# Optimization experiments

Measured on AMD Instinct MI355X. Metric: run time of the kernel, lower is better.

Reference implementation:

```python
import jax, jax.numpy as jnp
import numpy as np

D = 1024; H = 16; K = 64; BK = 32; FFN = 4096; LORA = 48; CHUNK = 64
THETA_CLIP = float(np.pi / 2)
THETA_INIT = float(np.pi / 16)


def layernorm(x, g, b, eps=1e-6):
    m = x.mean(-1, keepdims=True)
    v = ((x - m) ** 2).mean(-1, keepdims=True)
    return (x - m) * jax.lax.rsqrt(v + eps) * g + b


def setup_inputs() -> dict:
    key = jax.random.key(0)
    ks = jax.random.split(key, 24)
    w = lambda k, s: jax.random.normal(k, s, jnp.float32) * 0.02
    return {
        "x": jax.random.normal(ks[0], (4, 2048, D), jnp.float32),
        "Wq": w(ks[1], (D, D)), "bq": jnp.zeros((D,), jnp.float32),
        "Wk": w(ks[2], (D, D)), "bk": jnp.zeros((D,), jnp.float32),
        "Wv": w(ks[3], (D, D)), "bv": jnp.zeros((D,), jnp.float32),
        "Wo": w(ks[4], (D, D)), "bo": jnp.zeros((D,), jnp.float32),
        "n1g": jnp.ones((D,), jnp.float32), "n1b": jnp.zeros((D,), jnp.float32),
        "n2g": jnp.ones((D,), jnp.float32), "n2b": jnp.zeros((D,), jnp.float32),
        "theta_base": jax.random.uniform(ks[5], (H, BK), jnp.float32, -THETA_INIT, THETA_INIT),
        "theta_w1": w(ks[6], (D, LORA)),
        "theta_w2": jax.random.uniform(ks[7], (LORA, H * BK), jnp.float32, -0.01, 0.01),
        "lambda_base": jax.random.uniform(ks[8], (H, BK), jnp.float32, 0.5, 6.0),
        "eta": jax.random.normal(ks[9], (H, BK), jnp.float32) * 0.1,
        "Wf1": w(ks[10], (D, FFN)), "bf1": jnp.zeros((FFN,), jnp.float32),
        "Wf2": w(ks[11], (FFN, D)), "bf2": jnp.zeros((D,), jnp.float32),
    }


def _forward(x, Wq, bq, Wk, bk, Wv, bv, Wo, bo, n1g, n1b, n2g, n2b,
             theta_base, theta_w1, theta_w2, lambda_base, eta, Wf1, bf1, Wf2, bf2):
    B, T, _ = x.shape
    NC = T // CHUNK
    xn = layernorm(x, n1g, n1b)
    # projections -> (B, H, T, K)
    q = (xn @ Wq + bq).reshape(B, T, H, K).transpose(0, 2, 1, 3)
    k = (xn @ Wk + bk).reshape(B, T, H, K).transpose(0, 2, 1, 3)
    v = (xn @ Wv + bv).reshape(B, T, H, K).transpose(0, 2, 1, 3)
    phi_k = jnp.where(k > 0, k + 1.0, jnp.exp(k))  # elu(k) + 1
    qp = q.reshape(B, H, T, BK, 2)
    kp = phi_k.reshape(B, H, T, BK, 2)
    q_c = jax.lax.complex(qp[..., 0], qp[..., 1])  # (B,H,T,BK) complex64
    k_c = jax.lax.complex(kp[..., 0], kp[..., 1])
    # data-dependent rotation angles via LoRA
    lora = jnp.tanh(xn @ theta_w1) @ theta_w2  # (B,T,H*BK)
    theta = theta_base[None, None] + lora.reshape(B, T, H, BK)
    theta = jnp.clip(theta, -THETA_CLIP, THETA_CLIP).transpose(0, 2, 1, 3)  # (B,H,T,BK)
    lam = lambda_base[None, :, None, :] + eta[None, :, None, :] * theta ** 2
    log_z = jax.lax.complex(-lam, theta)  # complex log-decay per step

    def chunks(a):  # (B,H,T,...) -> (NC,B,H,CHUNK,...)
        return jnp.moveaxis(a.reshape(B, H, NC, CHUNK, *a.shape[3:]), 2, 0)

    tril = jnp.tril(jnp.ones((CHUNK, CHUNK), bool))[None, None, :, :, None]

    def step(c, inputs):
        lz, kc, qc, vf = inputs  # (B,H,tc,BK)x3, (B,H,tc,K)
        cumlog = jnp.cumsum(lz, axis=2)
        diff = cumlog[:, :, :, None, :] - cumlog[:, :, None, :, :]  # (B,H,tc,tc,BK)
        real = jnp.where(tril, diff.real, -60.0)
        A = jnp.where(tril, jnp.exp(jax.lax.complex(real, diff.imag)),
                      jnp.zeros((), jnp.complex64))
        scaled_k = A * kc[:, :, None, :, :]
        S_intra = jnp.einsum('bhtsk,bhsv->bhtkv', scaled_k, vf.astype(jnp.complex64))
        decay = jnp.exp(cumlog)
        S_total = decay[..., None] * c[:, :, None] + S_intra  # (B,H,tc,BK,K)
        y = jnp.einsum('bhtk,bhtkv->bhtv', jnp.conj(qc), S_total).real
        return S_total[:, :, -1], y

    c0 = jnp.zeros((B, H, BK, K), jnp.complex64)
    _, ys = jax.lax.scan(step, c0, (chunks(log_z), chunks(k_c), chunks(q_c), chunks(v)))
    out = jnp.moveaxis(ys, 0, 2).reshape(B, H, T, K)
    attn = out.transpose(0, 2, 1, 3).reshape(B, T, D) @ Wo + bo
    x1 = x + attn
    h = layernorm(x1, n2g, n2b)
    return x1 + jax.nn.gelu(h @ Wf1 + bf1) @ Wf2 + bf2


def reference(x, Wq, bq, Wk, bk, Wv, bv, Wo, bo, n1g, n1b, n2g, n2b,
              theta_base, theta_w1, theta_w2, lambda_base, eta, Wf1, bf1, Wf2, bf2):
    return _forward(x, Wq, bq, Wk, bk, Wv, bv, Wo, bo, n1g, n1b, n2g, n2b,
                    theta_base, theta_w1, theta_w2, lambda_base, eta, Wf1, bf1, Wf2, bf2)
```

## Files before the change

### kernel.cpp

```cpp
#include <hip/hip_runtime.h>


typedef __bf16 bf16x8 __attribute__((ext_vector_type(8)));
typedef float f32x4 __attribute__((ext_vector_type(4)));

__device__ __forceinline__ unsigned short f2bf(float f) {
  unsigned int u = __builtin_bit_cast(unsigned int, f);
  u += 0x7FFFu + ((u >> 16) & 1u);
  return (unsigned short)(u >> 16);
}
__device__ __forceinline__ float bf2f(unsigned short u) {
  unsigned int x = ((unsigned int)u) << 16;
  return __builtin_bit_cast(float, x);
}
__device__ __forceinline__ unsigned int pack2(float a, float b) {
  return (unsigned int)f2bf(a) | ((unsigned int)f2bf(b) << 16);
}

__device__ __forceinline__ void gload_lds16(const void* g, void* l) {
  __builtin_amdgcn_global_load_lds((const __attribute__((address_space(1))) void*)g,
                                   (__attribute__((address_space(3))) void*)l, 16, 0, 0);
}

__device__ __forceinline__ float gelu_tanh(float v) {
  const float z = 0.7978845608028654f * fmaf(0.044715f * v * v, v, v);
  const float e = __expf(2.f * z);
  return 0.5f * v * (2.f - 2.f / (1.f + e));
}

__global__ void fill_kernel(float* p, float v, int n) {
  int i = blockIdx.x * 256 + threadIdx.x;
  if (i < n) p[i] = v;
}

__global__ __launch_bounds__(256) void ln_kernel(
    const float* __restrict__ x, const float* __restrict__ g,
    const float* __restrict__ b, unsigned short* __restrict__ out) {
  const int row = blockIdx.x, tid = threadIdx.x;
  float4 v = ((const float4*)(x + (size_t)row * 1024))[tid];
  float s = v.x + v.y + v.z + v.w;
  float sq = v.x * v.x + v.y * v.y + v.z * v.z + v.w * v.w;
#pragma unroll
  for (int o = 32; o > 0; o >>= 1) { s += __shfl_xor(s, o); sq += __shfl_xor(sq, o); }
  __shared__ float red[8];
  const int wid = tid >> 6;
  if ((tid & 63) == 0) { red[wid] = s; red[4 + wid] = sq; }
  __syncthreads();
  s = red[0] + red[1] + red[2] + red[3];
  sq = red[4] + red[5] + red[6] + red[7];
  const float mean = s * (1.f / 1024.f);
  const float var = sq * (1.f / 1024.f) - mean * mean;
  const float rstd = rsqrtf(var + 1e-6f);
  float4 gv = ((const float4*)g)[tid];
  float4 bvv = ((const float4*)b)[tid];
  ushort4 o4;
  o4.x = f2bf((v.x - mean) * rstd * gv.x + bvv.x);
  o4.y = f2bf((v.y - mean) * rstd * gv.y + bvv.y);
  o4.z = f2bf((v.z - mean) * rstd * gv.z + bvv.z);
  o4.w = f2bf((v.w - mean) * rstd * gv.w + bvv.w);
  *(ushort4*)(out + (size_t)row * 1024 + tid * 4) = o4;
}

__global__ __launch_bounds__(256) void transpose_bf16(
    const float* __restrict__ src, unsigned short* __restrict__ dst, int K, int N) {
  __shared__ float tile[32][33];
  const int n0 = blockIdx.x * 32, k0 = blockIdx.y * 32;
  const int tx = threadIdx.x, ty = threadIdx.y;
#pragma unroll
  for (int j = 0; j < 32; j += 8) tile[tx][ty + j] = src[(size_t)(k0 + ty + j) * N + n0 + tx];
  __syncthreads();
#pragma unroll
  for (int j = 0; j < 32; j += 8)
    dst[(size_t)(n0 + ty + j) * K + k0 + tx] = f2bf(tile[ty + j][tx]);
}

__global__ __launch_bounds__(256) void prep_wcat(
    const float* __restrict__ Wq, const float* __restrict__ Wk,
    const float* __restrict__ Wv, const float* __restrict__ tw1,
    unsigned short* __restrict__ dst) {
  __shared__ float tile[32][33];
  const int r0 = blockIdx.x * 32, c0 = blockIdx.y * 32;
  const int tx = threadIdx.x, ty = threadIdx.y;
  const int r = r0 + tx;
#pragma unroll
  for (int j = 0; j < 32; j += 8) {
    const int c = c0 + ty + j;
    float v;
    if (r < 1024) v = Wq[(size_t)c * 1024 + r];
    else if (r < 2048) v = Wk[(size_t)c * 1024 + (r - 1024)];
    else if (r < 3072) v = Wv[(size_t)c * 1024 + (r - 2048)];
    else if (r < 3120) v = tw1[(size_t)c * 48 + (r - 3072)];
    else v = 0.f;
    tile[tx][ty + j] = v;
  }
  __syncthreads();
#pragma unroll
  for (int j = 0; j < 32; j += 8)
    dst[(size_t)(r0 + ty + j) * 1024 + c0 + tx] = f2bf(tile[ty + j][tx]);
}

__global__ void biascat_kernel(const float* bq, const float* bk, const float* bv, float* dst) {
  int i = blockIdx.x * 256 + threadIdx.x;
  if (i >= 3200) return;
  float v = 0.f;
  if (i < 1024) v = bq[i];
  else if (i < 2048) v = bk[i - 1024];
  else if (i < 3072) v = bv[i - 2048];
  dst[i] = v;
}

template <int MODE>
__global__ __launch_bounds__(256) void gemm_kernel(
    const unsigned short* __restrict__ A, const unsigned short* __restrict__ BT,
    const float* __restrict__ bias, const float* __restrict__ res,
    void* __restrict__ out, int N, int Kd) {
  __shared__ unsigned short As[128 * 64];
  __shared__ unsigned short Bs[128 * 64];
  const int nwg = gridDim.x * gridDim.y;
  int d = blockIdx.y * gridDim.x + blockIdx.x;
  d = (d & 7) * (nwg >> 3) + (d >> 3);
  const int n0 = (d % gridDim.x) * 128, m0 = (d / gridDim.x) * 128;

  const int tid = threadIdx.x, wv = tid >> 6, ln = tid & 63;
  const int wm = wv >> 1, wn = wv & 1;
  const int l15 = ln & 15, hi4 = ln >> 4;
  const int rbase = wv * 8 + (ln >> 3);
  const int kgofs = ((ln & 7) ^ ((ln >> 3) & 7)) * 8;

  f32x4 acc[4][4] = {};
  for (int k0 = 0; k0 < Kd; k0 += 64) {
#pragma unroll
    for (int jj = 0; jj < 4; ++jj) {
      gload_lds16(A + (size_t)(m0 + jj * 32 + rbase) * Kd + k0 + kgofs,
                  (char*)As + (jj * 256 + wv * 64) * 16);
      gload_lds16(BT + (size_t)(n0 + jj * 32 + rbase) * Kd + k0 + kgofs,
                  (char*)Bs + (jj * 256 + wv * 64) * 16);
    }
    __syncthreads();
#pragma unroll
    for (int kk = 0; kk < 64; kk += 32) {
      const int kg = (kk >> 3) + hi4;
      bf16x8 av[4], bv[4];
#pragma unroll
      for (int f = 0; f < 4; ++f) {
        const int ra = wm * 64 + f * 16 + l15;
        const int rb2 = wn * 64 + f * 16 + l15;
        av[f] = *(const bf16x8*)&As[(ra * 8 + (kg ^ (ra & 7))) * 8];
        bv[f] = *(const bf16x8*)&Bs[(rb2 * 8 + (kg ^ (rb2 & 7))) * 8];
      }
#pragma unroll
      for (int fm = 0; fm < 4; ++fm)
#pragma unroll
        for (int fn = 0; fn < 4; ++fn)
          acc[fm][fn] = __builtin_amdgcn_mfma_f32_16x16x32_bf16(av[fm], bv[fn], acc[fm][fn], 0, 0, 0);
    }
    __syncthreads();
  }
  const int rb = hi4 * 4;
#pragma unroll
  for (int fm = 0; fm < 4; ++fm) {
#pragma unroll
    for (int fn = 0; fn < 4; ++fn) {
      const int row = m0 + wm * 64 + fm * 16 + rb;
      const int col = n0 + wn * 64 + fn * 16 + l15;
      const float bval = bias[col];
#pragma unroll
      for (int r = 0; r < 4; ++r) {
        float v = acc[fm][fn][r] + bval;
        const size_t oi = (size_t)(row + r) * N + col;
        if constexpr (MODE == 1) v += res[oi];
        if constexpr (MODE == 2) {
          ((unsigned short*)out)[oi] = f2bf(gelu_tanh(v));
        } else if constexpr (MODE == 3) {
          ((unsigned short*)out)[oi] = f2bf(v);
        } else {
          ((float*)out)[oi] = v;
        }
      }
    }
  }
}

__global__ __launch_bounds__(256) void lora2_kernel(
    const unsigned short* __restrict__ qkv, const float* __restrict__ w2,
    const float* __restrict__ tbase, float* __restrict__ theta) {
  __shared__ float lt[8][48];
  const int m0 = blockIdx.x * 32;
  const int tid = threadIdx.x;
  const int col = tid * 2;
  const float tb0 = tbase[col], tb1 = tbase[col + 1];
  for (int grp = 0; grp < 4; ++grp) {
    const int mg = m0 + grp * 8;
    __syncthreads();
    for (int idx = tid; idx < 384; idx += 256) {
      const int tok = idx / 48, jj = idx % 48;
      lt[tok][jj] = tanhf(bf2f(qkv[(size_t)(mg + tok) * 3200 + 3072 + jj]));
    }
    __syncthreads();
    float a0[8], a1[8];
#pragma unroll
    for (int tok = 0; tok < 8; ++tok) { a0[tok] = tb0; a1[tok] = tb1; }
    for (int jj = 0; jj < 48; ++jj) {
      const float2 w = *(const float2*)&w2[(size_t)jj * 512 + col];
#pragma unroll
      for (int tok = 0; tok < 8; ++tok) {
        const float l = lt[tok][jj];
        a0[tok] = fmaf(l, w.x, a0[tok]);
        a1[tok] = fmaf(l, w.y, a1[tok]);
      }
    }
    const float CL = 1.5707963267948966f;
#pragma unroll
    for (int tok = 0; tok < 8; ++tok) {
      float c0 = fminf(fmaxf(a0[tok], -CL), CL);
      float c1 = fminf(fmaxf(a1[tok], -CL), CL);
      *(float2*)&theta[(size_t)(mg + tok) * 512 + col] = make_float2(c0, c1);
    }
  }
}

__global__ __launch_bounds__(256) void attn_intra(
    const unsigned short* __restrict__ qkv, const float* __restrict__ theta,
    const float* __restrict__ lamb, const float* __restrict__ eta,
    float* __restrict__ yi, unsigned short* __restrict__ QG,
    unsigned short* __restrict__ TCG, float* __restrict__ Dg) {
  const int c = blockIdx.x, bh = blockIdx.y;
  const int b = bh >> 4, h = bh & 15;
  const int tid = threadIdx.x, wv = tid >> 6, lane = tid & 63;
  const int sc = c * 4 + wv;
  const int cid = bh * 128 + sc;
  const int mw = b * 2048 + sc * 16;

  __shared__ unsigned short QDm[4][16][64];
  __shared__ unsigned short KDm[4][16][64];
  __shared__ unsigned short KdET[4][64][32];
  __shared__ unsigned short VT[4][64][32];
  __shared__ unsigned short Gs[4][16][32];

  {
    unsigned int* kz = (unsigned int*)&KdET[wv][0][0];
    unsigned int* vz = (unsigned int*)&VT[wv][0][0];
    for (int idx = lane; idx < 512; idx += 64) {
      const int r = idx >> 3, p = (idx & 7) + 8;
      kz[r * 16 + p] = 0; vz[r * 16 + p] = 0;
    }
    unsigned int* gz = (unsigned int*)&Gs[wv][0][0];
    for (int idx = lane; idx < 128; idx += 64) {
      const int r = idx >> 3, p = (idx & 7) + 8;
      gz[r * 16 + p] = 0;
    }
  }
  for (int ss = 0; ss < 16; ++ss)
    VT[wv][lane][ss] = qkv[(size_t)(mw + ss) * 3200 + 2048 + h * 64 + lane];

  const int bk = lane & 31, th = lane >> 5;
  const float lb = lamb[h * 32 + bk], et = eta[h * 32 + bk];
  float L[8], Th[8], qr[8], qi[8], kr[8], ki[8];
  float runL = 0.f, runT = 0.f;
#pragma unroll
  for (int i = 0; i < 8; ++i) {
    const size_t m = (size_t)(mw + th * 8 + i);
    const float tv = theta[m * 512 + h * 32 + bk];
    const float lam = fmaf(et * tv, tv, lb);
    runL += lam; L[i] = runL;
    runT += tv;  Th[i] = runT;
    const unsigned int qp = *(const unsigned int*)&qkv[m * 3200 + h * 64 + 2 * bk];
    const unsigned int kp = *(const unsigned int*)&qkv[m * 3200 + 1024 + h * 64 + 2 * bk];
    qr[i] = bf2f((unsigned short)(qp & 0xFFFF)); qi[i] = bf2f((unsigned short)(qp >> 16));
    const float kx = bf2f((unsigned short)(kp & 0xFFFF));
    const float ky = bf2f((unsigned short)(kp >> 16));
    kr[i] = kx > 0.f ? kx + 1.f : __expf(kx);
    ki[i] = ky > 0.f ? ky + 1.f : __expf(ky);
  }
  const float oL = __shfl_xor(runL, 32), oT = __shfl_xor(runT, 32);
  const float Lm = th ? oL : runL;
  const float Tm = th ? oT : runT;
  const float Ltot = runL + oL, Ttot = runT + oT;
  const float Lbase = th ? oL : 0.f, Tbase = th ? oT : 0.f;
  float Es, Ec; __sincosf(Tm, &Es, &Ec);
  const float Ee = __expf(-Lm);
  const float Er = Ee * Ec, Ei = Ee * Es;
  float Fs, Fc; __sincosf(Ttot - Tm, &Fs, &Fc);
  const float Fe = __expf(-(Ltot - Lm));
  const float Fr = Fe * Fc, Fi = Fe * Fs;
  if (th == 0) {
    float Ds, Dc; __sincosf(Ttot, &Ds, &Dc);
    const float De = __expf(-Ltot);
    *(float2*)&Dg[((size_t)cid * 32 + bk) * 2] = make_float2(De * Dc, De * Ds);
  }
  unsigned int* qd32 = (unsigned int*)&QDm[wv][0][0];
  unsigned int* kd32 = (unsigned int*)&KDm[wv][0][0];
#pragma unroll
  for (int i = 0; i < 8; ++i) {
    const int t = th * 8 + i;
    const float Lg = Lbase + L[i], Tg = Tbase + Th[i];
    const float dm = __expf(-(Lg - Lm));
    float sn, cs; __sincosf(Tg - Tm, &sn, &cs);
    const float qmr = dm * (qr[i] * cs + qi[i] * sn);
    const float qmi = dm * (qr[i] * sn - qi[i] * cs);
    const float rd = 1.f / dm;
    const float kmr = rd * (kr[i] * cs + ki[i] * sn);
    const float kmi = rd * (ki[i] * cs - kr[i] * sn);
    const int sidx = (t * 32 + bk) ^ ((t & 7) << 2);
    qd32[sidx] = pack2(qmr, qmi);
    kd32[sidx] = pack2(kmr, -kmi);
    ((unsigned int*)QG)[(size_t)cid * 512 + t * 32 + bk] =
        pack2(qmr * Er - qmi * Ei, qmr * Ei + qmi * Er);
    const float er = kmr * Fr - kmi * Fi;
    const float ei = kmr * Fi + kmi * Fr;
    KdET[wv][bk][t] = f2bf(er);
    KdET[wv][32 + bk][t] = f2bf(ei);
  }

  const int l15 = lane & 15, hi = lane >> 4;
  const char* qb = (const char*)&QDm[wv][0][0];
  const char* kb = (const char*)&KDm[wv][0][0];
  f32x4 z = {};
  f32x4 g = z;
  {
    bf16x8 a0 = *(const bf16x8*)(qb + l15 * 128 + ((16 * hi) ^ ((l15 & 7) << 4)));
    bf16x8 b0 = *(const bf16x8*)(kb + l15 * 128 + ((16 * hi) ^ ((l15 & 7) << 4)));
    bf16x8 a1 = *(const bf16x8*)(qb + l15 * 128 + ((64 + 16 * hi) ^ ((l15 & 7) << 4)));
    bf16x8 b1 = *(const bf16x8*)(kb + l15 * 128 + ((64 + 16 * hi) ^ ((l15 & 7) << 4)));
    g = __builtin_amdgcn_mfma_f32_16x16x32_bf16(a0, b0, g, 0, 0, 0);
    g = __builtin_amdgcn_mfma_f32_16x16x32_bf16(a1, b1, g, 0, 0, 0);
  }
#pragma unroll
  for (int r = 0; r < 4; ++r) {
    const float gv = (l15 <= 4 * hi + r) ? g[r] : 0.f;
    Gs[wv][4 * hi + r][l15] = f2bf(gv);
  }
  const char* gsb = (const char*)&Gs[wv][0][0];
  const char* vtb = (const char*)&VT[wv][0][0];
  bf16x8 aG = *(const bf16x8*)(gsb + l15 * 64 + 16 * hi);
#pragma unroll
  for (int nt = 0; nt < 4; ++nt) {
    bf16x8 bV = *(const bf16x8*)(vtb + (nt * 16 + l15) * 64 + 16 * hi);
    f32x4 y = __builtin_amdgcn_mfma_f32_16x16x32_bf16(aG, bV, z, 0, 0, 0);
#pragma unroll
    for (int r = 0; r < 4; ++r)
      yi[(size_t)cid * 1024 + (4 * hi + r) * 64 + nt * 16 + l15] = y[r];
  }
  const char* keb = (const char*)&KdET[wv][0][0];
#pragma unroll
  for (int mt = 0; mt < 4; ++mt) {
    bf16x8 aT = *(const bf16x8*)(keb + (mt * 16 + l15) * 64 + 16 * hi);
#pragma unroll
    for (int nt = 0; nt < 4; ++nt) {
      bf16x8 bV = *(const bf16x8*)(vtb + (nt * 16 + l15) * 64 + 16 * hi);
      f32x4 t4 = __builtin_amdgcn_mfma_f32_16x16x32_bf16(aT, bV, z, 0, 0, 0);
#pragma unroll
      for (int r = 0; r < 4; ++r)
        TCG[(size_t)cid * 4096 + (mt * 16 + 4 * hi + r) * 64 + nt * 16 + l15] = f2bf(t4[r]);
    }
  }
}

__global__ __launch_bounds__(256) void scanB_kernel(
    const unsigned short* __restrict__ TCG, const float* __restrict__ Dg,
    unsigned int* __restrict__ CPACK) {
  const int bh = blockIdx.x & 63, g = blockIdx.x >> 6;
  const int tid = threadIdx.x;
  const int v = g * 8 + (tid >> 5), bk = tid & 31;
  const size_t base = (size_t)bh * 128;
  float Cr = 0.f, Ci = 0.f;
  float trx[4], tix[4]; float2 dx[4];
  auto LOADQ = [&](int c0, float* tr, float* ti, float2* dd) {
#pragma unroll
    for (int u = 0; u < 4; ++u) {
      const size_t cid = base + c0 + u;
      tr[u] = bf2f(TCG[cid * 4096 + bk * 64 + v]);
      ti[u] = bf2f(TCG[cid * 4096 + (32 + bk) * 64 + v]);
      dd[u] = *(const float2*)&Dg[(cid * 32 + bk) * 2];
    }
  };
  LOADQ(0, trx, tix, dx);
  for (int c0 = 0; c0 < 128; c0 += 4) {
    float tra[4], tia[4]; float2 da[4];
#pragma unroll
    for (int u = 0; u < 4; ++u) { tra[u] = trx[u]; tia[u] = tix[u]; da[u] = dx[u]; }
    if (c0 + 4 < 128) LOADQ(c0 + 4, trx, tix, dx);
#pragma unroll
    for (int u = 0; u < 4; ++u) {
      CPACK[(base + c0 + u) * 2048 + v * 32 + bk] = pack2(Cr, -Ci);
      const float nr = fmaf(da[u].x, Cr, fmaf(-da[u].y, Ci, tra[u]));
      const float ni = fmaf(da[u].x, Ci, fmaf(da[u].y, Cr, tia[u]));
      Cr = nr; Ci = ni;
    }
  }
}

__global__ __launch_bounds__(256) void attn_cross(
    const float* __restrict__ yi, const unsigned short* __restrict__ QG,
    const unsigned int* __restrict__ CPACK, unsigned short* __restrict__ attn) {
  const int c = blockIdx.x, bh = blockIdx.y;
  const int b = bh >> 4, h = bh & 15;
  const int tid = threadIdx.x, wv = tid >> 6, lane = tid & 63;
  const int sc = c * 4 + wv, cid = bh * 128 + sc;
  const int mw = b * 2048 + sc * 16;
  __shared__ unsigned short Cp[4][64][64];
  __shared__ unsigned short Qs[4][16][64];
  unsigned int* cp32 = (unsigned int*)&Cp[wv][0][0];
  const unsigned int* cg = CPACK + (size_t)cid * 2048;
  for (int ii = 0; ii < 32; ++ii) {
    const int flat = ii * 64 + lane;
    const int row = flat >> 5, col = flat & 31;
    cp32[(row * 32 + col) ^ ((row & 7) << 2)] = cg[flat];
  }
  unsigned int* qs32 = (unsigned int*)&Qs[wv][0][0];
  const unsigned int* qg = (const unsigned int*)QG + (size_t)cid * 512;
  for (int ii = 0; ii < 8; ++ii) {
    const int flat = ii * 64 + lane;
    const int row = flat >> 5, col = flat & 31;
    qs32[(row * 32 + col) ^ ((row & 7) << 2)] = qg[flat];
  }
  const int l15 = lane & 15, hi = lane >> 4;
  const char* qb = (const char*)&Qs[wv][0][0];
  const char* cb = (const char*)&Cp[wv][0][0];
  bf16x8 a0 = *(const bf16x8*)(qb + l15 * 128 + ((16 * hi) ^ ((l15 & 7) << 4)));
  bf16x8 a1 = *(const bf16x8*)(qb + l15 * 128 + ((64 + 16 * hi) ^ ((l15 & 7) << 4)));
  f32x4 z = {};
#pragma unroll
  for (int nt = 0; nt < 4; ++nt) {
    const int vr = nt * 16 + l15;
    bf16x8 b0 = *(const bf16x8*)(cb + vr * 128 + ((16 * hi) ^ ((vr & 7) << 4)));
    bf16x8 b1 = *(const bf16x8*)(cb + vr * 128 + ((64 + 16 * hi) ^ ((vr & 7) << 4)));
    f32x4 y = __builtin_amdgcn_mfma_f32_16x16x32_bf16(a0, b0, z, 0, 0, 0);
    y = __builtin_amdgcn_mfma_f32_16x16x32_bf16(a1, b1, y, 0, 0, 0);
#pragma unroll
    for (int r = 0; r < 4; ++r) {
      const int t = 4 * hi + r;
      const float out = y[r] + yi[(size_t)cid * 1024 + t * 64 + vr];
      attn[(size_t)(mw + t) * 1024 + h * 64 + vr] = f2bf(out);
    }
  }
}

extern "C" void kernel_launch(void* const* d_in, const int* in_sizes, int n_in,
                              void* d_out, int out_size, void* d_ws, size_t ws_size,
                              hipStream_t stream) {
  const float* x   = (const float*)d_in[0];
  const float* Wq  = (const float*)d_in[1];
  const float* bq  = (const float*)d_in[2];
  const float* Wk  = (const float*)d_in[3];
  const float* bk_ = (const float*)d_in[4];
  const float* Wv  = (const float*)d_in[5];
  const float* bv  = (const float*)d_in[6];
  const float* Wo  = (const float*)d_in[7];
  const float* bo  = (const float*)d_in[8];
  const float* n1g = (const float*)d_in[9];
  const float* n1b = (const float*)d_in[10];
  const float* n2g = (const float*)d_in[11];
  const float* n2b = (const float*)d_in[12];
  const float* thb = (const float*)d_in[13];
  const float* tw1 = (const float*)d_in[14];
  const float* tw2 = (const float*)d_in[15];
  const float* lamb= (const float*)d_in[16];
  const float* eta = (const float*)d_in[17];
  const float* Wf1 = (const float*)d_in[18];
  const float* bf1 = (const float*)d_in[19];
  const float* Wf2 = (const float*)d_in[20];
  const float* bf2 = (const float*)d_in[21];

  char* ws = (char*)d_ws;
  size_t off = 0;
  auto alloc = [&](size_t bytes) {
    size_t r = off;
    off += (bytes + 255) & ~(size_t)255;
    return r;
  };
  unsigned short* WCAT = (unsigned short*)(ws + alloc(3200ull * 1024 * 2));
  unsigned short* WOT  = (unsigned short*)(ws + alloc(1024ull * 1024 * 2));
  unsigned short* WF1T = (unsigned short*)(ws + alloc(4096ull * 1024 * 2));
  unsigned short* WF2T = (unsigned short*)(ws + alloc(1024ull * 4096 * 2));
  float* BIASC = (float*)(ws + alloc(3200ull * 4));
  unsigned short* XN = (unsigned short*)(ws + alloc(8192ull * 1024 * 2));
  char* QKVbase = ws + alloc(8192ull * 4096 * 2);
  unsigned short* QKV = (unsigned short*)QKVbase;
  unsigned int* CPACK = (unsigned int*)QKVbase;
  unsigned short* GBUF = (unsigned short*)QKVbase;
  float* THETA = (float*)(ws + alloc(8192ull * 512 * 4));
  unsigned short* ATTN = (unsigned short*)THETA;
  float* YI = (float*)(ws + alloc(8192ull * 1024 * 4));
  float* X1 = YI;
  unsigned short* QG = (unsigned short*)(ws + alloc(8192ull * 1024 * 2));
  unsigned short* TCG = (unsigned short*)(ws + alloc(8192ull * 4096 * 2));
  float* DG = (float*)(ws + alloc(8192ull * 32 * 2 * 4));

  if (ws_size < off) {
    fill_kernel<<<dim3((out_size + 255) / 256), dim3(256), 0, stream>>>((float*)d_out, 12345.0f, out_size);
    return;
  }

  const dim3 b256(256), b32x8(32, 8);

  prep_wcat<<<dim3(100, 32), b32x8, 0, stream>>>(Wq, Wk, Wv, tw1, WCAT);
  transpose_bf16<<<dim3(32, 32), b32x8, 0, stream>>>(Wo, WOT, 1024, 1024);
  transpose_bf16<<<dim3(128, 32), b32x8, 0, stream>>>(Wf1, WF1T, 1024, 4096);
  transpose_bf16<<<dim3(32, 128), b32x8, 0, stream>>>(Wf2, WF2T, 4096, 1024);
  biascat_kernel<<<dim3(13), b256, 0, stream>>>(bq, bk_, bv, BIASC);

  ln_kernel<<<dim3(8192), b256, 0, stream>>>(x, n1g, n1b, XN);
  gemm_kernel<3><<<dim3(25, 64), b256, 0, stream>>>(XN, WCAT, BIASC, nullptr, QKV, 3200, 1024);
  lora2_kernel<<<dim3(256), b256, 0, stream>>>(QKV, tw2, thb, THETA);
  attn_intra<<<dim3(32, 64), b256, 0, stream>>>(QKV, THETA, lamb, eta, YI, QG, TCG, DG);
  scanB_kernel<<<dim3(512), b256, 0, stream>>>(TCG, DG, CPACK);
  attn_cross<<<dim3(32, 64), b256, 0, stream>>>(YI, QG, CPACK, ATTN);
  gemm_kernel<1><<<dim3(8, 64), b256, 0, stream>>>(ATTN, WOT, bo, x, X1, 1024, 1024);
  ln_kernel<<<dim3(8192), b256, 0, stream>>>(X1, n2g, n2b, XN);
  gemm_kernel<2><<<dim3(32, 64), b256, 0, stream>>>(XN, WF1T, bf1, nullptr, GBUF, 4096, 1024);
  gemm_kernel<1><<<dim3(8, 64), b256, 0, stream>>>(GBUF, WF2T, bf2, X1, d_out, 1024, 4096);
}
```

Measured before the change: 520.9 us.

## Add 256x256 eight-wave pipelined GEMM with split-K for FFN down-projection

Adds a 512-thread GEMM kernel with 256x256 output tiles. It uses double-buffered LDS filled by direct global-to-LDS loads with an XOR swizzle, staggers the B-tile prefetch across the compute phases, and raises MFMA priority around the math. The QKV, FFN-up and FFN-down GEMMs move to this kernel. The QKV width is padded from 3200 to 3328 so it divides into 256-wide tiles. FFN-down uses a 2-way split-K into a scratch buffer that reuses the TCG workspace, followed by a reduce kernel that adds the bias and residual. The aim is more data reuse per tile and better latency hiding, at the cost of some padded work, extra partial-sum traffic and one more kernel launch.

```diff
diff --git a/kernel.cpp b/kernel.cpp
--- a/kernel.cpp
+++ b/kernel.cpp
@@ -1,5 +1,7 @@
 #include <hip/hip_runtime.h>
 
+
+#define QS 3328
 
 typedef __bf16 bf16x8 __attribute__((ext_vector_type(8)));
 typedef float f32x4 __attribute__((ext_vector_type(4)));
@@ -101,7 +103,7 @@
 
 __global__ void biascat_kernel(const float* bq, const float* bk, const float* bv, float* dst) {
   int i = blockIdx.x * 256 + threadIdx.x;
-  if (i >= 3200) return;
+  if (i >= QS) return;
   float v = 0.f;
   if (i < 1024) v = bq[i];
   else if (i < 2048) v = bk[i - 1024];
@@ -169,16 +171,148 @@
         float v = acc[fm][fn][r] + bval;
         const size_t oi = (size_t)(row + r) * N + col;
         if constexpr (MODE == 1) v += res[oi];
+        ((float*)out)[oi] = v;
+      }
+    }
+  }
+}
+
+template <int MODE>
+__global__ __launch_bounds__(512, 2) void gemm8p_kernel(
+    const unsigned short* __restrict__ A, const unsigned short* __restrict__ BT,
+    const float* __restrict__ bias, void* __restrict__ out,
+    int N, int Kstride, int Klen) {
+  __shared__ __align__(16) unsigned short SA[2][2][8192];
+  __shared__ __align__(16) unsigned short SB[2][2][8192];
+  const int nwg = gridDim.x * gridDim.y;
+  int d = blockIdx.y * gridDim.x + blockIdx.x;
+  d = (d & 7) * (nwg >> 3) + (d >> 3);
+  const int n0 = (d % gridDim.x) * 256, m0 = (d / gridDim.x) * 256;
+  const int koff = blockIdx.z * Klen;
+
+  const int tid = threadIdx.x, wv = tid >> 6, ln = tid & 63;
+  const int wm = wv >> 2, wn = wv & 3;
+  const int l15 = ln & 15, hi4 = ln >> 4;
+
+  const unsigned short* Abase = A + (size_t)m0 * Kstride + koff;
+  const unsigned short* Bbase = BT + (size_t)n0 * Kstride + koff;
+
+  const int srow = (ln >> 3);
+  const int skg = (ln & 7);
+  auto SHALF = [&](char* sbuf, const unsigned short* base, int h, int k0) {
+#pragma unroll
+    for (int r = 0; r < 2; ++r) {
+      const int row = (r * 8 + wv) * 8 + srow;
+      const int kg = skg ^ (row & 7);
+      gload_lds16(base + (size_t)(h * 128 + row) * Kstride + k0 + kg * 8,
+                  sbuf + h * 16384 + (r * 8 + wv) * 1024);
+    }
+  };
+
+  f32x4 acc[8][4] = {};
+  const int nt = Klen >> 6;
+  SHALF((char*)&SA[0][0][0], Abase, 0, 0);
+  SHALF((char*)&SA[0][0][0], Abase, 1, 0);
+  SHALF((char*)&SB[0][0][0], Bbase, 0, 0);
+  SHALF((char*)&SB[0][0][0], Bbase, 1, 0);
+  SHALF((char*)&SA[1][0][0], Abase, 0, 64);
+  SHALF((char*)&SA[1][0][0], Abase, 1, 64);
+  asm volatile("s_waitcnt vmcnt(4)" ::: "memory");
+  __builtin_amdgcn_s_barrier();
+
+  for (int t = 0; t < nt; ++t) {
+    const int p = t & 1;
+    const unsigned short* Ah = &SA[p][wm][0];
+    const unsigned short* Bh = &SB[p][wn >> 1][0];
+    const int brow_base = (wn & 1) * 64;
+    bf16x8 bfr[4][2];
+#pragma unroll
+    for (int q = 0; q < 4; ++q) {
+      bf16x8 af[2][2];
+#pragma unroll
+      for (int j = 0; j < 2; ++j) {
+        const int row = (2 * q + j) * 16 + l15;
+#pragma unroll
+        for (int ks = 0; ks < 2; ++ks) {
+          const int kg = ks * 4 + hi4;
+          af[j][ks] = *(const bf16x8*)&Ah[(row * 8 + (kg ^ (row & 7))) * 8];
+        }
+      }
+      if (q == 0) {
+#pragma unroll
+        for (int fn = 0; fn < 4; ++fn) {
+          const int rowb = brow_base + fn * 16 + l15;
+#pragma unroll
+          for (int ks = 0; ks < 2; ++ks) {
+            const int kg = ks * 4 + hi4;
+            bfr[fn][ks] = *(const bf16x8*)&Bh[(rowb * 8 + (kg ^ (rowb & 7))) * 8];
+          }
+        }
+      }
+      if (q < 2 && t + 1 < nt)
+        SHALF((char*)&SB[p ^ 1][0][0], Bbase, q, (t + 1) << 6);
+      __builtin_amdgcn_s_setprio(1);
+#pragma unroll
+      for (int j = 0; j < 2; ++j)
+#pragma unroll
+        for (int fn = 0; fn < 4; ++fn)
+#pragma unroll
+          for (int ks = 0; ks < 2; ++ks)
+            acc[2 * q + j][fn] = __builtin_amdgcn_mfma_f32_16x16x32_bf16(
+                af[j][ks], bfr[fn][ks], acc[2 * q + j][fn], 0, 0, 0);
+      __builtin_amdgcn_s_setprio(0);
+      __builtin_amdgcn_s_barrier();
+    }
+    if (t + 2 < nt) {
+      SHALF((char*)&SA[p][0][0], Abase, 0, (t + 2) << 6);
+      SHALF((char*)&SA[p][0][0], Abase, 1, (t + 2) << 6);
+    }
+    if (t + 1 < nt) {
+      if (t + 2 < nt) asm volatile("s_waitcnt vmcnt(4)" ::: "memory");
+      else            asm volatile("s_waitcnt vmcnt(0)" ::: "memory");
+      __builtin_amdgcn_s_barrier();
+    }
+  }
+
+#pragma unroll
+  for (int fm = 0; fm < 8; ++fm) {
+#pragma unroll
+    for (int fn = 0; fn < 4; ++fn) {
+      const int row = m0 + wm * 128 + fm * 16 + hi4 * 4;
+      const int col = n0 + wn * 64 + fn * 16 + l15;
+      float bval = 0.f;
+      if constexpr (MODE != 4) bval = bias[col];
+#pragma unroll
+      for (int r = 0; r < 4; ++r) {
+        const float v = acc[fm][fn][r] + bval;
+        const size_t oi = (size_t)(row + r) * N + col;
         if constexpr (MODE == 2) {
           ((unsigned short*)out)[oi] = f2bf(gelu_tanh(v));
         } else if constexpr (MODE == 3) {
           ((unsigned short*)out)[oi] = f2bf(v);
         } else {
-          ((float*)out)[oi] = v;
+          ((float*)out)[(size_t)blockIdx.z * 8192 * 1024 + oi] = v;
         }
       }
     }
   }
+}
+
+__global__ __launch_bounds__(256) void reduce2_kernel(
+    const float* __restrict__ p0, const float* __restrict__ p1,
+    const float* __restrict__ bias, const float* __restrict__ res,
+    float* __restrict__ out) {
+  const size_t i = ((size_t)blockIdx.x * 256 + threadIdx.x) * 4;
+  float4 a = *(const float4*)&p0[i];
+  float4 b = *(const float4*)&p1[i];
+  float4 r = *(const float4*)&res[i];
+  float4 bv = *(const float4*)&bias[i & 1023];
+  float4 o;
+  o.x = a.x + b.x + r.x + bv.x;
+  o.y = a.y + b.y + r.y + bv.y;
+  o.z = a.z + b.z + r.z + bv.z;
+  o.w = a.w + b.w + r.w + bv.w;
+  *(float4*)&out[i] = o;
 }
 
 __global__ __launch_bounds__(256) void lora2_kernel(
@@ -194,7 +328,7 @@
     __syncthreads();
     for (int idx = tid; idx < 384; idx += 256) {
       const int tok = idx / 48, jj = idx % 48;
-      lt[tok][jj] = tanhf(bf2f(qkv[(size_t)(mg + tok) * 3200 + 3072 + jj]));
+      lt[tok][jj] = tanhf(bf2f(qkv[(size_t)(mg + tok) * QS + 3072 + jj]));
     }
     __syncthreads();
     float a0[8], a1[8];
@@ -251,7 +385,7 @@
     }
   }
   for (int ss = 0; ss < 16; ++ss)
-    VT[wv][lane][ss] = qkv[(size_t)(mw + ss) * 3200 + 2048 + h * 64 + lane];
+    VT[wv][lane][ss] = qkv[(size_t)(mw + ss) * QS + 2048 + h * 64 + lane];
 
   const int bk = lane & 31, th = lane >> 5;
   const float lb = lamb[h * 32 + bk], et = eta[h * 32 + bk];
@@ -264,8 +398,8 @@
     const float lam = fmaf(et * tv, tv, lb);
     runL += lam; L[i] = runL;
     runT += tv;  Th[i] = runT;
-    const unsigned int qp = *(const unsigned int*)&qkv[m * 3200 + h * 64 + 2 * bk];
-    const unsigned int kp = *(const unsigned int*)&qkv[m * 3200 + 1024 + h * 64 + 2 * bk];
+    const unsigned int qp = *(const unsigned int*)&qkv[m * QS + h * 64 + 2 * bk];
+    const unsigned int kp = *(const unsigned int*)&qkv[m * QS + 1024 + h * 64 + 2 * bk];
     qr[i] = bf2f((unsigned short)(qp & 0xFFFF)); qi[i] = bf2f((unsigned short)(qp >> 16));
     const float kx = bf2f((unsigned short)(kp & 0xFFFF));
     const float ky = bf2f((unsigned short)(kp >> 16));
@@ -469,11 +603,11 @@
     off += (bytes + 255) & ~(size_t)255;
     return r;
   };
-  unsigned short* WCAT = (unsigned short*)(ws + alloc(3200ull * 1024 * 2));
+  unsigned short* WCAT = (unsigned short*)(ws + alloc((size_t)QS * 1024 * 2));
   unsigned short* WOT  = (unsigned short*)(ws + alloc(1024ull * 1024 * 2));
   unsigned short* WF1T = (unsigned short*)(ws + alloc(4096ull * 1024 * 2));
   unsigned short* WF2T = (unsigned short*)(ws + alloc(1024ull * 4096 * 2));
-  float* BIASC = (float*)(ws + alloc(3200ull * 4));
+  float* BIASC = (float*)(ws + alloc((size_t)QS * 4));
   unsigned short* XN = (unsigned short*)(ws + alloc(8192ull * 1024 * 2));
   char* QKVbase = ws + alloc(8192ull * 4096 * 2);
   unsigned short* QKV = (unsigned short*)QKVbase;
@@ -484,7 +618,9 @@
   float* YI = (float*)(ws + alloc(8192ull * 1024 * 4));
   float* X1 = YI;
   unsigned short* QG = (unsigned short*)(ws + alloc(8192ull * 1024 * 2));
-  unsigned short* TCG = (unsigned short*)(ws + alloc(8192ull * 4096 * 2));
+  char* TCGbase = ws + alloc(8192ull * 4096 * 2);
+  unsigned short* TCG = (unsigned short*)TCGbase;
+  float* PART = (float*)TCGbase;
   float* DG = (float*)(ws + alloc(8192ull * 32 * 2 * 4));
 
   if (ws_size < off) {
@@ -492,22 +628,23 @@
     return;
   }
 
-  const dim3 b256(256), b32x8(32, 8);
-
-  prep_wcat<<<dim3(100, 32), b32x8, 0, stream>>>(Wq, Wk, Wv, tw1, WCAT);
+  const dim3 b256(256), b32x8(32, 8), b512(512);
+
+  prep_wcat<<<dim3(104, 32), b32x8, 0, stream>>>(Wq, Wk, Wv, tw1, WCAT);
   transpose_bf16<<<dim3(32, 32), b32x8, 0, stream>>>(Wo, WOT, 1024, 1024);
   transpose_bf16<<<dim3(128, 32), b32x8, 0, stream>>>(Wf1, WF1T, 1024, 4096);
   transpose_bf16<<<dim3(32, 128), b32x8, 0, stream>>>(Wf2, WF2T, 4096, 1024);
   biascat_kernel<<<dim3(13), b256, 0, stream>>>(bq, bk_, bv, BIASC);
 
   ln_kernel<<<dim3(8192), b256, 0, stream>>>(x, n1g, n1b, XN);
-  gemm_kernel<3><<<dim3(25, 64), b256, 0, stream>>>(XN, WCAT, BIASC, nullptr, QKV, 3200, 1024);
+  gemm8p_kernel<3><<<dim3(13, 32), b512, 0, stream>>>(XN, WCAT, BIASC, QKV, QS, 1024, 1024);
   lora2_kernel<<<dim3(256), b256, 0, stream>>>(QKV, tw2, thb, THETA);
   attn_intra<<<dim3(32, 64), b256, 0, stream>>>(QKV, THETA, lamb, eta, YI, QG, TCG, DG);
   scanB_kernel<<<dim3(512), b256, 0, stream>>>(TCG, DG, CPACK);
   attn_cross<<<dim3(32, 64), b256, 0, stream>>>(YI, QG, CPACK, ATTN);
   gemm_kernel<1><<<dim3(8, 64), b256, 0, stream>>>(ATTN, WOT, bo, x, X1, 1024, 1024);
   ln_kernel<<<dim3(8192), b256, 0, stream>>>(X1, n2g, n2b, XN);
-  gemm_kernel<2><<<dim3(32, 64), b256, 0, stream>>>(XN, WF1T, bf1, nullptr, GBUF, 4096, 1024);
-  gemm_kernel<1><<<dim3(8, 64), b256, 0, stream>>>(GBUF, WF2T, bf2, X1, d_out, 1024, 4096);
-}
+  gemm8p_kernel<2><<<dim3(16, 32), b512, 0, stream>>>(XN, WF1T, bf1, GBUF, 4096, 1024, 1024);
+  gemm8p_kernel<4><<<dim3(4, 32, 2), b512, 0, stream>>>(GBUF, WF2T, nullptr, PART, 1024, 4096, 2048);
+  reduce2_kernel<<<dim3(8192), b256, 0, stream>>>(PART, PART + 8192ull * 1024, bf2, X1, (float*)d_out);
+}
```

New measurement: 501.6 us. 1.04x faster.
